# Kernel optimization log

Hardware: AMD Instinct MI355X
Metric: run time of the kernel (lower is better)

## Reference

```python
import jax, jax.numpy as jnp
import numpy as np

S, E, H = 4096, 1024, 16
D = E // H
N_SEG = 64


def setup_inputs() -> dict:
    key = jax.random.key(0)
    ks = jax.random.split(key, 11)
    scale = 0.02
    inp = {
        "x": jax.random.normal(ks[0], (S, E), dtype=jnp.float32),
        "Wq": jax.random.normal(ks[1], (E, E), dtype=jnp.float32) * scale,
        "bq": jax.random.normal(ks[2], (E,), dtype=jnp.float32) * scale,
        "Wk": jax.random.normal(ks[3], (E, E), dtype=jnp.float32) * scale,
        "bk": jax.random.normal(ks[4], (E,), dtype=jnp.float32) * scale,
        "Wv": jax.random.normal(ks[5], (E, E), dtype=jnp.float32) * scale,
        "bv": jax.random.normal(ks[6], (E,), dtype=jnp.float32) * scale,
        "Wo": jax.random.normal(ks[7], (E, E), dtype=jnp.float32) * scale,
        "bo": jax.random.normal(ks[8], (E,), dtype=jnp.float32) * scale,
        "segment_ids": jnp.sort(jax.random.randint(ks[9], (S,), 0, N_SEG)).astype(jnp.int32),
        "pos": 100,
    }
    return inp


def reference(x, Wq, bq, Wk, bk, Wv, bv, Wo, bo, segment_ids, pos):
    # torch Linear: y = x @ W.T + b
    q = (x @ Wq.T + bq).reshape(S, H, D)  # [S, H, D]
    k = (x @ Wk.T + bk).reshape(S, H, D)
    v = (x @ Wv.T + bv).reshape(S, H, D)

    # same-segment mask (contiguous segments from gene-structure dividers)
    mask = segment_ids[:, None] == segment_ids[None, :]  # [S, S]

    # NOTE: original leaves out-of-segment scores at 0 (not -inf) and applies
    # softmax over the FULL row; also no 1/sqrt(d) scaling. Reproduce exactly.
    scores = jnp.einsum("shd,thd->hst", q, k)            # [H, S, S]
    scores = jnp.where(mask[None, :, :], scores, 0.0)
    weights = jax.nn.softmax(scores, axis=-1)            # softmax over full row

    wv = jnp.einsum("hst,thd->shd", weights, v).reshape(S, E)
    out = wv @ Wo.T + bo                                  # [S, E]

    # mean over the main context: tokens sharing pos's segment
    main = (segment_ids == segment_ids[pos]).astype(out.dtype)  # [S]
    result = (out * main[:, None]).sum(axis=0) / main.sum()
    return result
```

## Files before the change

kernel.cpp:

```cpp
#include <hip/hip_runtime.h>
#include <math.h>

#define SS 4096
#define EE 1024
#define HH 16
#define DD 64
#define RMAX 128
#define NCOL 128
#define NTR  8
#define NRED 8
#define NPROJ 1536
#define NBG 64
#define NVS 16
#define NATT 256

#define OFF_SUMX  64
#define OFF_BGA   1088
#define OFF_BETA  2112
#define OFF_ALPHA 3136
#define OFF_VSUM  3200
#define OFF_PART  8192
#define OFF_XT    (OFF_PART + EE * NCOL)
#define OFF_QH    (OFF_XT + EE * RMAX)
#define OFF_KTH   (OFF_QH + HH * RMAX * DD)
#define OFF_VH    (OFF_KTH + HH * DD * RMAX)

__device__ __forceinline__ void seg_scan(const int* __restrict__ seg,
                                         const int* __restrict__ posp,
                                         int* sh, int& s0, int& L) {
    if (threadIdx.x == 0) { sh[0] = SS; sh[1] = -1; }
    __syncthreads();
    int sid = seg[posp[0]];
    int lmin = SS, lmax = -1;
    for (int i = threadIdx.x; i < SS; i += 256)
        if (seg[i] == sid) { lmin = min(lmin, i); lmax = max(lmax, i); }
#pragma unroll
    for (int off = 32; off; off >>= 1) {
        lmin = min(lmin, __shfl_xor(lmin, off));
        lmax = max(lmax, __shfl_xor(lmax, off));
    }
    if ((threadIdx.x & 63) == 0) { atomicMin(&sh[0], lmin); atomicMax(&sh[1], lmax); }
    __syncthreads();
    s0 = sh[0];
    L  = sh[1] - sh[0] + 1;
    if (L > RMAX) L = RMAX;
    if (L < 1)    L = 1;
}

__global__ __launch_bounds__(256) void d0_kernel(
    const float* __restrict__ x, const int* __restrict__ seg,
    const int* __restrict__ posp, float* __restrict__ ws) {
    int bid = blockIdx.x, tid = threadIdx.x;
    if (bid < NCOL) {
        float* partT = ws + OFF_PART;
        int r0 = bid * (SS / NCOL);
        const float4* x4 = (const float4*)x;
        float4 a = make_float4(0.f, 0.f, 0.f, 0.f);
#pragma unroll 8
        for (int r = 0; r < SS / NCOL; ++r) {
            float4 v = x4[(size_t)(r0 + r) * 256 + tid];
            a.x += v.x; a.y += v.y; a.z += v.z; a.w += v.w;
        }
        partT[(size_t)(4 * tid + 0) * NCOL + bid] = a.x;
        partT[(size_t)(4 * tid + 1) * NCOL + bid] = a.y;
        partT[(size_t)(4 * tid + 2) * NCOL + bid] = a.z;
        partT[(size_t)(4 * tid + 3) * NCOL + bid] = a.w;
        return;
    }
    __shared__ float t[128 * 129];
    __shared__ int sh[2];
    int s0, L;
    seg_scan(seg, posp, sh, s0, L);
    int kb = bid - NCOL;
    if (kb == 0 && tid == 0) { ((int*)ws)[0] = s0; ((int*)ws)[1] = L; }
    int k0 = kb * 128;
    float* xT = ws + OFF_XT;
    for (int idx = tid; idx < 128 * 32; idx += 256) {
        int r = idx >> 5, c4 = idx & 31;
        float4 v = make_float4(0.f, 0.f, 0.f, 0.f);
        if (r < L) v = *(const float4*)(x + (size_t)(s0 + r) * EE + k0 + c4 * 4);
        t[r * 129 + c4 * 4 + 0] = v.x;
        t[r * 129 + c4 * 4 + 1] = v.y;
        t[r * 129 + c4 * 4 + 2] = v.z;
        t[r * 129 + c4 * 4 + 3] = v.w;
    }
    __syncthreads();
    for (int idx = tid; idx < 128 * 32; idx += 256) {
        int k = idx >> 5, r4 = idx & 31;
        float4 o;
        o.x = t[(r4 * 4 + 0) * 129 + k];
        o.y = t[(r4 * 4 + 1) * 129 + k];
        o.z = t[(r4 * 4 + 2) * 129 + k];
        o.w = t[(r4 * 4 + 3) * 129 + k];
        *(float4*)(xT + (size_t)(k0 + k) * RMAX + r4 * 4) = o;
    }
}

__global__ __launch_bounds__(256) void d1_kernel(
    const float* __restrict__ Wq, const float* __restrict__ bq,
    const float* __restrict__ Wk, const float* __restrict__ bk,
    const float* __restrict__ Wv, const float* __restrict__ bv,
    float* __restrict__ ws) {
    int bid = blockIdx.x, tid = threadIdx.x;
    if (bid < NRED) {
        if (bid == 0) {
            for (int i = tid; i < 1088; i += 256) (ws + OFF_BETA)[i] = 0.f;
        }
        const float* partT = ws + OFF_PART;
        int e  = bid * 128 + (tid >> 1);
        int c0 = (tid & 1) * 64;
        const float4* p4 = (const float4*)(partT + (size_t)e * NCOL + c0);
        float4 s4 = make_float4(0.f, 0.f, 0.f, 0.f);
#pragma unroll
        for (int i = 0; i < 16; ++i) {
            float4 v = p4[i];
            s4.x += v.x; s4.y += v.y; s4.z += v.z; s4.w += v.w;
        }
        float s = s4.x + s4.y + s4.z + s4.w;
        s += __shfl_xor(s, 1);
        if ((tid & 1) == 0) (ws + OFF_SUMX)[e] = s;
        return;
    }
    __shared__ float red[16 * 66];
    int L  = ((const int*)ws)[1];
    int Lp = (L + 63) & ~63;
    int pid = bid - NRED;
    int m   = pid / 512;
    int rem = pid - m * 512;
    int eb  = rem >> 1;
    int rt  = rem & 1;
    int r0  = rt * 64;
    if (r0 >= Lp) return;
    int e0 = eb * 4;
    const float* W = (m == 0) ? Wq : ((m == 1) ? Wk : Wv);
    const float* b = (m == 0) ? bq : ((m == 1) ? bk : bv);
    int lane = tid & 63;
    int w4 = __builtin_amdgcn_readfirstlane(tid >> 6);
    const float* xcol = ws + OFF_XT + r0 + lane;
    int kbase = w4 * 256;
    const float* wr0 = W + (size_t)e0 * EE + kbase;
    float acc0 = 0.f, acc1 = 0.f, acc2 = 0.f, acc3 = 0.f;
    float xv0[8], xv1[8];
#pragma unroll
    for (int u = 0; u < 8; ++u) xv0[u] = xcol[(size_t)(kbase + u) * RMAX];
    for (int kk = 0; kk < 256; kk += 16) {
#pragma unroll
        for (int u = 0; u < 8; ++u)
            xv1[u] = xcol[(size_t)(kbase + kk + 8 + u) * RMAX];
#pragma unroll
        for (int u = 0; u < 8; ++u) {
            float w0 = wr0[0 * EE + kk + u];
            float w1 = wr0[1 * EE + kk + u];
            float w2 = wr0[2 * EE + kk + u];
            float w3 = wr0[3 * EE + kk + u];
            acc0 += xv0[u] * w0; acc1 += xv0[u] * w1;
            acc2 += xv0[u] * w2; acc3 += xv0[u] * w3;
        }
#pragma unroll
        for (int u = 0; u < 8; ++u)
            xv0[u] = xcol[(size_t)(kbase + kk + 16 + u) * RMAX];
#pragma unroll
        for (int u = 0; u < 8; ++u) {
            float w0 = wr0[0 * EE + kk + 8 + u];
            float w1 = wr0[1 * EE + kk + 8 + u];
            float w2 = wr0[2 * EE + kk + 8 + u];
            float w3 = wr0[3 * EE + kk + 8 + u];
            acc0 += xv1[u] * w0; acc1 += xv1[u] * w1;
            acc2 += xv1[u] * w2; acc3 += xv1[u] * w3;
        }
    }
    red[(w4 * 4 + 0) * 66 + lane] = acc0;
    red[(w4 * 4 + 1) * 66 + lane] = acc1;
    red[(w4 * 4 + 2) * 66 + lane] = acc2;
    red[(w4 * 4 + 3) * 66 + lane] = acc3;
    __syncthreads();
    int p  = tid >> 6;
    int rg = r0 + lane;
    float* qh  = ws + OFF_QH;
    float* kTh = ws + OFF_KTH;
    float* vh  = ws + OFF_VH;
    int h = e0 >> 6, d0 = (e0 & 63) + p;
    float v = 0.f;
    if (rg < L)
        v = red[(0 * 4 + p) * 66 + lane] + red[(1 * 4 + p) * 66 + lane]
          + red[(2 * 4 + p) * 66 + lane] + red[(3 * 4 + p) * 66 + lane]
          + b[e0 + p];
    if (m == 1) kTh[(size_t)(h * DD + d0) * RMAX + rg] = v;
    else        ((m == 0) ? qh : vh)[((size_t)h * RMAX + rg) * DD + d0] = v;
}

__global__ __launch_bounds__(256) void d2_kernel(
    const float* __restrict__ Wv, const float* __restrict__ bv,
    float* __restrict__ ws) {
    __shared__ float qS[4 * 64];
    __shared__ float wS[4 * 128];
    __shared__ float vp_[4][64];
    const float* sumx = ws + OFF_SUMX;
    float* bgA    = ws + OFF_BGA;
    float* betap  = ws + OFF_BETA;
    float* alphap = ws + OFF_ALPHA;
    float* vsumh  = ws + OFF_VSUM;
    const float* qh  = ws + OFF_QH;
    const float* kTh = ws + OFF_KTH;
    const float* vh  = ws + OFF_VH;

    int bid = blockIdx.x, tid = threadIdx.x;
    int lane = tid & 63, wave = tid >> 6;
    int L  = ((const int*)ws)[1];
    int Lp = (L + 63) & ~63;

    if (bid < NBG) {
        int e = bid * 16 + (tid >> 4);
        int j = tid & 15;
        const float4* wr  = (const float4*)(Wv + (size_t)e * EE);
        const float4* sx4 = (const float4*)sumx;
        float p = 0.f;
#pragma unroll
        for (int jj = 0; jj < 16; ++jj) {
            float4 w = wr[jj * 16 + j], z = sx4[jj * 16 + j];
            p += w.x * z.x + w.y * z.y + w.z * z.z + w.w * z.w;
        }
        p += __shfl_xor(p, 8);
        p += __shfl_xor(p, 4);
        p += __shfl_xor(p, 2);
        p += __shfl_xor(p, 1);
        if (j == 0) bgA[e] = p + (float)SS * bv[e];
        return;
    }
    if (bid < NBG + NVS) {
        int h = bid - NBG;
        float s = 0.f;
        for (int t = wave; t < Lp; t += 4)
            s += vh[((size_t)h * RMAX + t) * DD + lane];
        vp_[wave][lane] = s;
        __syncthreads();
        if (wave == 0)
            vsumh[h * DD + lane] = vp_[0][lane] + vp_[1][lane]
                                 + vp_[2][lane] + vp_[3][lane];
        return;
    }

    int aid = bid - NBG - NVS;
    int gidbase = aid * 4 + wave;
    int pairs = L * HH;
    float* qSw = qS + wave * 64;
    float* wSw = wS + wave * 128;
    for (int wg = gidbase; wg < pairs; wg += NATT * 4) {
        int h = wg & (HH - 1);
        int r = wg >> 4;
        qSw[lane] = qh[((size_t)h * RMAX + r) * DD + lane];
        float s0 = 0.f, s1 = 0.f;
#pragma unroll
        for (int d = 0; d < 64; ++d) {
            float qd = qSw[d];
            const float* kr = kTh + (size_t)(h * DD + d) * RMAX;
            s0 += qd * kr[lane];
            s1 += qd * kr[64 + lane];
        }
        float v0 = (lane < L)      ? s0 : -3.0e38f;
        float v1 = (64 + lane < L) ? s1 : -3.0e38f;
        float m = fmaxf(0.f, fmaxf(v0, v1));
#pragma unroll
        for (int off = 32; off; off >>= 1) m = fmaxf(m, __shfl_xor(m, off));
        float w0 = (lane < L)      ? __expf(s0 - m) : 0.f;
        float w1 = (64 + lane < L) ? __expf(s1 - m) : 0.f;
        float Zl = w0 + w1;
#pragma unroll
        for (int off = 32; off; off >>= 1) Zl += __shfl_xor(Zl, off);
        float em = __expf(-m);
        float Z  = Zl + (float)(SS - L) * em;
        wSw[lane]      = w0;
        wSw[64 + lane] = w1;
        float acc = 0.f;
#pragma unroll 16
        for (int t = 0; t < Lp; ++t)
            acc += wSw[t] * vh[((size_t)h * RMAX + t) * DD + lane];
        float invZ = 1.0f / Z;
        atomicAdd(&betap[h * DD + lane], acc * invZ);
        if (lane == 0) atomicAdd(&alphap[h], em * invZ);
    }
}

__global__ __launch_bounds__(256) void d3_kernel(
    const float* __restrict__ Wo, const float* __restrict__ bo,
    const float* __restrict__ ws, float* __restrict__ out) {
    __shared__ float z[EE];
    int tid = threadIdx.x;
    int lane = tid & 63, wave = tid >> 6;
    int L = ((const int*)ws)[1];

    {
        int h = tid >> 4;
        float4 beta = ((const float4*)(ws + OFF_BETA))[tid];
        float  a    = (ws + OFF_ALPHA)[h];
        float4 g    = ((const float4*)(ws + OFF_BGA))[tid];
        float4 vs   = ((const float4*)(ws + OFF_VSUM))[tid];
        ((float4*)z)[tid] = make_float4(beta.x + a * (g.x - vs.x),
                                        beta.y + a * (g.y - vs.y),
                                        beta.z + a * (g.z - vs.z),
                                        beta.w + a * (g.w - vs.w));
    }
    __syncthreads();

    int e = blockIdx.x * 4 + wave;
    const float4* wr = (const float4*)(Wo + (size_t)e * EE);
    const float4* z4 = (const float4*)z;
    float p = 0.f;
#pragma unroll
    for (int it = 0; it < 4; ++it) {
        float4 w = wr[it * 64 + lane], zz = z4[it * 64 + lane];
        p += w.x * zz.x + w.y * zz.y + w.z * zz.z + w.w * zz.w;
    }
#pragma unroll
    for (int off = 32; off; off >>= 1) p += __shfl_xor(p, off);
    if (lane == 0) out[e] = bo[e] + p / (float)L;
}

extern "C" void kernel_launch(void* const* d_in, const int* in_sizes, int n_in,
                              void* d_out, int out_size, void* d_ws, size_t ws_size,
                              hipStream_t stream) {
    const float* x   = (const float*)d_in[0];
    const float* Wq  = (const float*)d_in[1];
    const float* bq  = (const float*)d_in[2];
    const float* Wk  = (const float*)d_in[3];
    const float* bk  = (const float*)d_in[4];
    const float* Wv  = (const float*)d_in[5];
    const float* bv  = (const float*)d_in[6];
    const float* Wo  = (const float*)d_in[7];
    const float* bo  = (const float*)d_in[8];
    const int*   seg = (const int*)d_in[9];
    const int*   pos = (const int*)d_in[10];
    float*       out = (float*)d_out;
    float*       ws  = (float*)d_ws;

    d0_kernel<<<NCOL + NTR, 256, 0, stream>>>(x, seg, pos, ws);
    d1_kernel<<<NRED + NPROJ, 256, 0, stream>>>(Wq, bq, Wk, bk, Wv, bv, ws);
    d2_kernel<<<NBG + NVS + NATT, 256, 0, stream>>>(Wv, bv, ws);
    d3_kernel<<<EE / 4, 256, 0, stream>>>(Wo, bo, ws, out);
}
```

Baseline: 74.02 us.

## Stage projection weight rows in shared memory and cover both row tiles per block

Result: faster. 71.57 us (-3.3%).

```diff
diff --git a/kernel.cpp b/kernel.cpp
--- a/kernel.cpp
+++ b/kernel.cpp
@@ -9,7 +9,7 @@
 #define NCOL 128
 #define NTR  8
 #define NRED 8
-#define NPROJ 1536
+#define NPROJ 768
 #define NBG 64
 #define NVS 16
 #define NATT 256
@@ -121,72 +121,74 @@
         if ((tid & 1) == 0) (ws + OFF_SUMX)[e] = s;
         return;
     }
+    __shared__ float wsL[4 * EE];
     __shared__ float red[16 * 66];
     int L  = ((const int*)ws)[1];
     int Lp = (L + 63) & ~63;
+    int nh = Lp >> 6;
     int pid = bid - NRED;
-    int m   = pid / 512;
-    int rem = pid - m * 512;
-    int eb  = rem >> 1;
-    int rt  = rem & 1;
-    int r0  = rt * 64;
-    if (r0 >= Lp) return;
-    int e0 = eb * 4;
+    int m   = pid >> 8;
+    int eb  = pid & 255;
+    int e0  = eb * 4;
     const float* W = (m == 0) ? Wq : ((m == 1) ? Wk : Wv);
     const float* b = (m == 0) ? bq : ((m == 1) ? bk : bv);
+
+    {
+        const float4* src = (const float4*)(W + (size_t)e0 * EE);
+        float4* dst = (float4*)wsL;
+#pragma unroll
+        for (int i = 0; i < 4; ++i) dst[tid + i * 256] = src[tid + i * 256];
+    }
+    __syncthreads();
+
     int lane = tid & 63;
-    int w4 = __builtin_amdgcn_readfirstlane(tid >> 6);
-    const float* xcol = ws + OFF_XT + r0 + lane;
+    int w4   = tid >> 6;
     int kbase = w4 * 256;
-    const float* wr0 = W + (size_t)e0 * EE + kbase;
-    float acc0 = 0.f, acc1 = 0.f, acc2 = 0.f, acc3 = 0.f;
-    float xv0[8], xv1[8];
-#pragma unroll
-    for (int u = 0; u < 8; ++u) xv0[u] = xcol[(size_t)(kbase + u) * RMAX];
-    for (int kk = 0; kk < 256; kk += 16) {
+    const float* x0 = ws + OFF_XT + lane;
+    float acc[2][4] = {{0.f, 0.f, 0.f, 0.f}, {0.f, 0.f, 0.f, 0.f}};
+    for (int kk = 0; kk < 256; kk += 8) {
+        float xv0[8], xv1[8];
 #pragma unroll
         for (int u = 0; u < 8; ++u)
-            xv1[u] = xcol[(size_t)(kbase + kk + 8 + u) * RMAX];
-#pragma unroll
-        for (int u = 0; u < 8; ++u) {
-            float w0 = wr0[0 * EE + kk + u];
-            float w1 = wr0[1 * EE + kk + u];
-            float w2 = wr0[2 * EE + kk + u];
-            float w3 = wr0[3 * EE + kk + u];
-            acc0 += xv0[u] * w0; acc1 += xv0[u] * w1;
-            acc2 += xv0[u] * w2; acc3 += xv0[u] * w3;
-        }
-#pragma unroll
-        for (int u = 0; u < 8; ++u)
-            xv0[u] = xcol[(size_t)(kbase + kk + 16 + u) * RMAX];
-#pragma unroll
-        for (int u = 0; u < 8; ++u) {
-            float w0 = wr0[0 * EE + kk + 8 + u];
-            float w1 = wr0[1 * EE + kk + 8 + u];
-            float w2 = wr0[2 * EE + kk + 8 + u];
-            float w3 = wr0[3 * EE + kk + 8 + u];
-            acc0 += xv1[u] * w0; acc1 += xv1[u] * w1;
-            acc2 += xv1[u] * w2; acc3 += xv1[u] * w3;
-        }
-    }
-    red[(w4 * 4 + 0) * 66 + lane] = acc0;
-    red[(w4 * 4 + 1) * 66 + lane] = acc1;
-    red[(w4 * 4 + 2) * 66 + lane] = acc2;
-    red[(w4 * 4 + 3) * 66 + lane] = acc3;
-    __syncthreads();
-    int p  = tid >> 6;
-    int rg = r0 + lane;
+            xv0[u] = x0[(size_t)(kbase + kk + u) * RMAX];
+        if (nh == 2) {
+#pragma unroll
+            for (int u = 0; u < 8; ++u)
+                xv1[u] = x0[(size_t)(kbase + kk + u) * RMAX + 64];
+        }
+#pragma unroll
+        for (int j = 0; j < 4; ++j) {
+            const float4* wp = (const float4*)&wsL[j * EE + kbase + kk];
+            float4 wa = wp[0], wb = wp[1];
+            acc[0][j] += wa.x * xv0[0] + wa.y * xv0[1] + wa.z * xv0[2] + wa.w * xv0[3]
+                       + wb.x * xv0[4] + wb.y * xv0[5] + wb.z * xv0[6] + wb.w * xv0[7];
+            if (nh == 2)
+                acc[1][j] += wa.x * xv1[0] + wa.y * xv1[1] + wa.z * xv1[2] + wa.w * xv1[3]
+                           + wb.x * xv1[4] + wb.y * xv1[5] + wb.z * xv1[6] + wb.w * xv1[7];
+        }
+    }
+
     float* qh  = ws + OFF_QH;
     float* kTh = ws + OFF_KTH;
     float* vh  = ws + OFF_VH;
-    int h = e0 >> 6, d0 = (e0 & 63) + p;
-    float v = 0.f;
-    if (rg < L)
-        v = red[(0 * 4 + p) * 66 + lane] + red[(1 * 4 + p) * 66 + lane]
-          + red[(2 * 4 + p) * 66 + lane] + red[(3 * 4 + p) * 66 + lane]
-          + b[e0 + p];
-    if (m == 1) kTh[(size_t)(h * DD + d0) * RMAX + rg] = v;
-    else        ((m == 0) ? qh : vh)[((size_t)h * RMAX + rg) * DD + d0] = v;
+    int h = e0 >> 6;
+    for (int h2 = 0; h2 < nh; ++h2) {
+        __syncthreads();
+#pragma unroll
+        for (int j = 0; j < 4; ++j)
+            red[(w4 * 4 + j) * 66 + lane] = acc[h2][j];
+        __syncthreads();
+        int p  = w4;
+        int rg = h2 * 64 + lane;
+        float v = 0.f;
+        if (rg < L)
+            v = red[(0 * 4 + p) * 66 + lane] + red[(1 * 4 + p) * 66 + lane]
+              + red[(2 * 4 + p) * 66 + lane] + red[(3 * 4 + p) * 66 + lane]
+              + b[e0 + p];
+        int d0 = (e0 & 63) + p;
+        if (m == 1) kTh[(size_t)(h * DD + d0) * RMAX + rg] = v;
+        else        ((m == 0) ? qh : vh)[((size_t)h * RMAX + rg) * DD + d0] = v;
+    }
 }
 
 __global__ __launch_bounds__(256) void d2_kernel(
```
